# Optimization experiments

Hardware: AMD Instinct MI355X
Metric: run time of the kernel (lower is better)

Reference implementation:

```python
import jax, jax.numpy as jnp
import numpy as np

B, C, H, W = 4, 512, 64, 64
KEY_DIM, VALUE_DIM = 512, 512


def setup_inputs() -> dict:
    key = jax.random.key(0)
    k1, k2, k3, k4 = jax.random.split(key, 4)
    s = 1.0 / np.sqrt(C).astype(np.float32)
    x = jax.random.normal(k1, (B, C, H, W), jnp.float32)
    # torch nn.Linear weights have shape (out_features, in_features)
    Wk = jax.random.normal(k2, (KEY_DIM, C), jnp.float32) * s
    Wq = jax.random.normal(k3, (KEY_DIM, C), jnp.float32) * s
    Wv = jax.random.normal(k4, (VALUE_DIM, C), jnp.float32) * s
    return {"x": x, "Wk": Wk, "Wq": Wq, "Wv": Wv}


def reference(x, Wk, Wq, Wv):
    b, c, h, w = x.shape
    kd = Wk.shape[0]
    n = h * w
    # (b,c,h,w) -> (b, n, c) tokens, matching transpose+flatten in the original
    xt = x.transpose(0, 2, 3, 1).reshape(b, n, c)
    q = xt @ Wq.T  # (b, n, kd)
    k = xt @ Wk.T  # (b, n, kd)
    v = xt @ Wv.T  # (b, n, vd)
    scaling = np.sqrt(float(kd)).astype(np.float32)
    scores = jax.nn.softmax(jnp.einsum('bnd,bmd->bnm', q, k) / scaling, axis=-1)
    # original: output[j] = sum_i values[i] * scores[j, i]  ==  scores @ V
    out = jnp.einsum('bnm,bmv->bnv', scores, v)  # (b, n, vd)
    # original scores_out: sum over dim=0 (query index) of the (n, n) score matrix
    scores_out = scores.sum(axis=1).reshape(b, 1, h, w)
    out = out.reshape(b, h, w, -1).transpose(0, 3, 1, 2)  # (b, vd, h, w)
    return out, scores_out
```

## Files before the change

### kernel.cpp

```cpp
#include <hip/hip_runtime.h>


typedef short bf16x8 __attribute__((ext_vector_type(8)));
typedef float f32x4 __attribute__((ext_vector_type(4)));

#define NTOK 4096
#define DDIM 512
#define NB   4

__device__ __forceinline__ unsigned short f32_bf16(float f) {
  union { float f; unsigned u; } v; v.f = f;
  unsigned r = v.u + 0x7FFFu + ((v.u >> 16) & 1u);
  return (unsigned short)(r >> 16);
}

__device__ __forceinline__ float bf16_f32(short s) {
  union { unsigned u; float f; } v;
  v.u = ((unsigned)(unsigned short)s) << 16;
  return v.f;
}

__device__ __forceinline__ void gload_lds16(const unsigned short* g,
                                            unsigned short* l) {
  __builtin_amdgcn_global_load_lds(
      (__attribute__((address_space(1))) void*)(g),
      (__attribute__((address_space(3))) void*)(l), 16, 0, 0);
}

__global__ __launch_bounds__(256, 4) void qkv_proj(
    const float* __restrict__ x,
    const float* __restrict__ Wq,
    const float* __restrict__ Wk,
    const float* __restrict__ Wv,
    unsigned short* __restrict__ Qt,
    unsigned short* __restrict__ Kf,
    unsigned short* __restrict__ Vt)
{
  const int nt0 = blockIdx.x * 64;
  const int d0  = blockIdx.y * 64;
  const int b   = blockIdx.z;
  const int tid = threadIdx.x;
  const int wave = tid >> 6;
  const int lane = tid & 63;
  const int l15  = lane & 15;
  const int quad = lane >> 4;

  __shared__ __align__(16) unsigned short Xt[64 * 40];
  __shared__ __align__(16) unsigned short Wl[3][64 * 40];

  f32x4 aq[4], ak[4], av[4];
#pragma unroll
  for (int i = 0; i < 4; ++i) {
    aq[i] = (f32x4){0.f,0.f,0.f,0.f};
    ak[i] = (f32x4){0.f,0.f,0.f,0.f};
    av[i] = (f32x4){0.f,0.f,0.f,0.f};
  }

  const float* xb = x + (size_t)b * DDIM * NTOK + nt0;
  const int xn  = tid & 63;
  const int xc8 = tid >> 6;
  const int wc8 = tid & 3;
  const int wdd = tid >> 2;

  for (int cc = 0; cc < DDIM; cc += 32) {
    __syncthreads();
    {
      bf16x8 t;
#pragma unroll
      for (int j = 0; j < 8; ++j)
        t[j] = (short)f32_bf16(xb[(size_t)(cc + xc8 * 8 + j) * NTOK + xn]);
      *(bf16x8*)(&Xt[xn * 40 + xc8 * 8]) = t;
    }
    {
      const float* wsrc[3] = {Wq, Wk, Wv};
#pragma unroll
      for (int m = 0; m < 3; ++m) {
        const float* src = wsrc[m] + (size_t)(d0 + wdd) * DDIM + cc + wc8 * 8;
        bf16x8 t;
#pragma unroll
        for (int j = 0; j < 8; ++j) t[j] = (short)f32_bf16(src[j]);
        *(bf16x8*)(&Wl[m][wdd * 40 + wc8 * 8]) = t;
      }
    }
    __syncthreads();

    bf16x8 xa  = *(const bf16x8*)(&Xt[(wave * 16 + l15) * 40 + quad * 8]);
    bf16x8 wva = *(const bf16x8*)(&Wl[2][(wave * 16 + l15) * 40 + quad * 8]);
#pragma unroll
    for (int nt = 0; nt < 4; ++nt) {
      bf16x8 wqf = *(const bf16x8*)(&Wl[0][(nt * 16 + l15) * 40 + quad * 8]);
      bf16x8 wkf = *(const bf16x8*)(&Wl[1][(nt * 16 + l15) * 40 + quad * 8]);
      bf16x8 xbf = *(const bf16x8*)(&Xt[(nt * 16 + l15) * 40 + quad * 8]);
      aq[nt] = __builtin_amdgcn_mfma_f32_16x16x32_bf16(xa,  wqf, aq[nt], 0, 0, 0);
      ak[nt] = __builtin_amdgcn_mfma_f32_16x16x32_bf16(xa,  wkf, ak[nt], 0, 0, 0);
      av[nt] = __builtin_amdgcn_mfma_f32_16x16x32_bf16(wva, xbf, av[nt], 0, 0, 0);
    }
  }

#pragma unroll
  for (int nt = 0; nt < 4; ++nt) {
#pragma unroll
    for (int r = 0; r < 4; ++r) {
      const int tokq = nt0 + wave * 16 + quad * 4 + r;
      const int dq   = d0 + nt * 16 + l15;
      Qt[((size_t)b * NTOK + tokq) * DDIM + dq] = f32_bf16(aq[nt][r]);
      {
        const int kblk  = (nt0 >> 4) + wave;
        const int dc    = (d0 >> 5) + (nt >> 1);
        const int laneK = ((nt & 1) * 2 + (l15 >> 3)) * 16 + quad * 4 + r;
        Kf[((size_t)(b * 256 + kblk) * 16 + dc) * 512 + laneK * 8 + (l15 & 7)] =
            f32_bf16(ak[nt][r]);
      }
      const int dblk  = (d0 >> 4) + wave;
      const int ic    = (nt0 >> 5) + (nt >> 1);
      const int laneV = ((nt & 1) * 2 + (l15 >> 3)) * 16 + quad * 4 + r;
      Vt[(size_t)b * DDIM * NTOK +
         ((size_t)(dblk * 128 + ic) * 64 + laneV) * 8 + (l15 & 7)] =
          f32_bf16(av[nt][r]);
    }
  }
}

#define SCALE 0.044194173824159216f

__global__ __launch_bounds__(256, 2) void attn_lsum_p(
    const unsigned short* __restrict__ Qt,
    const unsigned short* __restrict__ Kf,
    unsigned short* __restrict__ Pt,
    float* __restrict__ lsum_g)
{
  const int qb = blockIdx.x;
  const int kp = blockIdx.y;
  const int b  = blockIdx.z;
  const int tid  = threadIdx.x;
  const int wave = tid >> 6;
  const int lane = tid & 63;
  const int l15  = lane & 15;
  const int quad = lane >> 4;
  const int q0   = qb * 128 + wave * 32;

  __shared__ __align__(16) unsigned short Klds[2][16384];

  bf16x8 qf[2][16];
#pragma unroll
  for (int qt = 0; qt < 2; ++qt) {
    const unsigned short* qp =
        Qt + ((size_t)b * NTOK + q0 + qt * 16 + l15) * DDIM + quad * 8;
#pragma unroll
    for (int dc = 0; dc < 16; ++dc) qf[qt][dc] = *(const bf16x8*)(qp + dc * 32);
  }

  unsigned short* Pq = Pt + (size_t)b * NTOK * NTOK +
                       (size_t)(qb * 2 + (wave >> 1)) * 262144;
  const int ntb = (wave & 1) * 2;

  float ls[2][4] = {{0.f,0.f,0.f,0.f},{0.f,0.f,0.f,0.f}};

  const unsigned short* Ksrc0 = Kf + ((size_t)(b * 256 + kp * 64) * 16) * 512;

#define KSTAGE(KC_, B_)                                                        \
  do {                                                                         \
    const unsigned short* ks_ = Ksrc0 + (size_t)(KC_)*16384;                   \
    _Pragma("unroll") for (int c_ = 0; c_ < 8; ++c_) {                         \
      const int ch_ = c_ * 4 + wave;                                           \
      gload_lds16(ks_ + ch_ * 512 + lane * 8, &Klds[B_][ch_ * 512]);           \
    }                                                                          \
  } while (0)

  KSTAGE(0, 0);
  __syncthreads();

  for (int kc2 = 0; kc2 < 32; ++kc2) {
    const int cb = kc2 & 1;
    if (kc2 < 31) KSTAGE(kc2 + 1, cb ^ 1);

#pragma unroll
    for (int kt = 0; kt < 2; ++kt) {
      const int kabs = kp * 64 + kc2 * 2 + kt;
      f32x4 s0 = (f32x4){0.f,0.f,0.f,0.f};
      f32x4 s1 = (f32x4){0.f,0.f,0.f,0.f};
#pragma unroll
      for (int dc = 0; dc < 16; ++dc) {
        const bf16x8 kbf =
            *(const bf16x8*)(&Klds[cb][(kt * 16 + dc) * 512 + lane * 8]);
        s0 = __builtin_amdgcn_mfma_f32_16x16x32_bf16(qf[0][dc], kbf, s0, 0, 0, 0);
        s1 = __builtin_amdgcn_mfma_f32_16x16x32_bf16(qf[1][dc], kbf, s1, 0, 0, 0);
      }
      const int ic    = kabs >> 1;
      const int lt_hi = ((kabs & 1) * 2 + (l15 >> 3)) * 16;
      const int jj    = l15 & 7;
#pragma unroll
      for (int r = 0; r < 4; ++r) {
        const float e0 = __expf(s0[r] * SCALE);
        const float e1 = __expf(s1[r] * SCALE);
        ls[0][r] += e0;
        ls[1][r] += e1;
        Pq[((size_t)(ic * 4 + ntb) * 64 + lt_hi + quad * 4 + r) * 8 + jj] =
            f32_bf16(e0);
        Pq[((size_t)(ic * 4 + ntb + 1) * 64 + lt_hi + quad * 4 + r) * 8 + jj] =
            f32_bf16(e1);
      }
    }
    __syncthreads();
  }
#undef KSTAGE

#pragma unroll
  for (int qt = 0; qt < 2; ++qt)
#pragma unroll
    for (int r = 0; r < 4; ++r) {
      float v = ls[qt][r];
      v += __shfl_xor(v, 1);
      v += __shfl_xor(v, 2);
      v += __shfl_xor(v, 4);
      v += __shfl_xor(v, 8);
      if (l15 == 0)
        unsafeAtomicAdd(&lsum_g[(size_t)b * NTOK + q0 + qt * 16 + quad * 4 + r], v);
    }
}

__global__ __launch_bounds__(256, 4) void attn_pv(
    const unsigned short* __restrict__ Pt,
    const unsigned short* __restrict__ Vt,
    const float* __restrict__ lsum_g,
    float* __restrict__ out,
    float* __restrict__ scpart)
{
  const int g     = blockIdx.x;
  const int xcd   = g & 7;
  const int slot  = g >> 3;
  const int combo = (xcd << 1) | (slot >> 6);
  const int q0b   = slot & 63;
  const int dpart = combo & 3;
  const int b     = combo >> 2;
  const int tid  = threadIdx.x;
  const int wave = tid >> 6;
  const int lane = tid & 63;
  const int l15  = lane & 15;
  const int quad = lane >> 4;

  const int dblk0 = dpart * 8 + wave * 2;
  const unsigned short* Pq =
      Pt + (size_t)b * NTOK * NTOK + (size_t)q0b * 262144;
  const unsigned short* Vb =
      Vt + (size_t)b * DDIM * NTOK + lane * 8;
  float* scp = scpart + ((size_t)(b * 64 + q0b)) * NTOK;

  __shared__ __align__(16) unsigned short Plds[2][8192];

  float rlv[4];
#pragma unroll
  for (int nt = 0; nt < 4; ++nt)
    rlv[nt] = 1.0f / lsum_g[(size_t)b * NTOK + q0b * 64 + nt * 16 + l15];

  f32x4 o[2][4];
#pragma unroll
  for (int i = 0; i < 2; ++i)
#pragma unroll
    for (int j = 0; j < 4; ++j) o[i][j] = (f32x4){0.f,0.f,0.f,0.f};

  bf16x8 vA[2], vB[2];

#define LOADVN(D_, IC_)                                                        \
  do {                                                                         \
    _Pragma("unroll") for (int mt = 0; mt < 2; ++mt)                           \
      D_[mt] = *(const bf16x8*)(Vb + (size_t)(dblk0 + mt) * 65536 +            \
                                (size_t)(IC_)*512);                            \
  } while (0)

#define PSTAGE(S_, B_)                                                         \
  do {                                                                         \
    const unsigned short* ps_ = Pq + (size_t)(S_)*8192;                        \
    _Pragma("unroll") for (int c_ = 0; c_ < 4; ++c_) {                         \
      const int ch_ = c_ * 4 + wave;                                           \
      gload_lds16(ps_ + ch_ * 512 + lane * 8, &Plds[B_][ch_ * 512]);           \
    }                                                                          \
  } while (0)

  LOADVN(vA, 0);
  LOADVN(vB, 1);
  PSTAGE(0, 0);
  __syncthreads();

  for (int s = 0; s < 32; ++s) {
    const int cb = s & 1;
    if (s < 31) PSTAGE(s + 1, cb ^ 1);
    const bool own = ((s >> 3) == dpart);
#pragma unroll
    for (int i = 0; i < 4; ++i) {
      const int ic = s * 4 + i;
      bf16x8 pb[4];
#pragma unroll
      for (int nt = 0; nt < 4; ++nt)
        pb[nt] = *(const bf16x8*)(&Plds[cb][i * 2048 + nt * 512 + lane * 8]);
      if ((i & 1) == 0) {
#pragma unroll
        for (int mt = 0; mt < 2; ++mt)
#pragma unroll
          for (int nt = 0; nt < 4; ++nt)
            o[mt][nt] = __builtin_amdgcn_mfma_f32_16x16x32_bf16(
                vA[mt], pb[nt], o[mt][nt], 0, 0, 0);
        if (ic + 2 < 128) LOADVN(vA, ic + 2);
      } else {
#pragma unroll
        for (int mt = 0; mt < 2; ++mt)
#pragma unroll
          for (int nt = 0; nt < 4; ++nt)
            o[mt][nt] = __builtin_amdgcn_mfma_f32_16x16x32_bf16(
                vB[mt], pb[nt], o[mt][nt], 0, 0, 0);
        if (ic + 2 < 128) LOADVN(vB, ic + 2);
      }
      if (own) {
#pragma unroll
        for (int jo = 0; jo < 2; ++jo) {
          const int j = wave * 2 + jo;
          float c = 0.f;
#pragma unroll
          for (int nt = 0; nt < 4; ++nt)
            c = fmaf(bf16_f32(pb[nt][j]), rlv[nt], c);
          c += __shfl_xor(c, 1);
          c += __shfl_xor(c, 2);
          c += __shfl_xor(c, 4);
          c += __shfl_xor(c, 8);
          if (l15 == 0) scp[ic * 32 + quad * 8 + j] = c;
        }
      }
    }
    __syncthreads();
  }
#undef LOADVN
#undef PSTAGE

  float* ob = out + ((size_t)b * DDIM + dpart * 128 + wave * 32) * NTOK + q0b * 64;
#pragma unroll
  for (int mt = 0; mt < 2; ++mt)
#pragma unroll
    for (int nt = 0; nt < 4; ++nt)
#pragma unroll
      for (int r = 0; r < 4; ++r)
        ob[(size_t)(mt * 16 + quad * 4 + r) * NTOK + nt * 16 + l15] =
            o[mt][nt][r] * rlv[nt];
}

__global__ __launch_bounds__(256, 8) void colsum_reduce(
    const float* __restrict__ scpart,
    float* __restrict__ scores_out)
{
  const int b = blockIdx.y;
  const int i = blockIdx.x * 256 + threadIdx.x;
  const float* src = scpart + (size_t)b * 64 * NTOK + i;
  float s = 0.f;
#pragma unroll
  for (int q = 0; q < 64; ++q) s += src[(size_t)q * NTOK];
  scores_out[(size_t)b * NTOK + i] = s;
}

extern "C" void kernel_launch(void* const* d_in, const int* in_sizes, int n_in,
                              void* d_out, int out_size, void* d_ws, size_t ws_size,
                              hipStream_t stream) {
  const float* x  = (const float*)d_in[0];
  const float* Wk = (const float*)d_in[1];
  const float* Wq = (const float*)d_in[2];
  const float* Wv = (const float*)d_in[3];

  float* out = (float*)d_out;
  float* scores_out = out + (size_t)NB * DDIM * NTOK;

  const size_t mat_elems = (size_t)NB * NTOK * DDIM;
  unsigned short* Qt = (unsigned short*)d_ws;
  unsigned short* Kf = Qt + mat_elems;
  unsigned short* Vt = Kf + mat_elems;
  float* lbuf = (float*)(Vt + mat_elems);
  unsigned short* Pt = (unsigned short*)(lbuf + (size_t)NB * NTOK);
  float* scpart = (float*)(Pt + (size_t)NB * NTOK * NTOK);

  hipMemsetAsync(lbuf, 0, (size_t)NB * NTOK * sizeof(float), stream);

  dim3 g1(NTOK / 64, DDIM / 64, NB);
  qkv_proj<<<g1, 256, 0, stream>>>(x, Wq, Wk, Wv, Qt, Kf, Vt);

  dim3 g2(NTOK / 128, 4, NB);
  attn_lsum_p<<<g2, 256, 0, stream>>>(Qt, Kf, Pt, lbuf);

  attn_pv<<<dim3(1024), 256, 0, stream>>>(Pt, Vt, lbuf, out, scpart);

  colsum_reduce<<<dim3(NTOK / 256, NB), 256, 0, stream>>>(scpart, scores_out);
}
```

Before: 355.2 us.

## Pre-convert inputs to bf16 token-major buffers and hoist column-sum out of PV loop

Adds a conversion kernel that transposes x to token-major bf16 and converts the weights to bf16 once, staging both in the P scratch buffer. The QKV projection then uses vectorized 16-byte loads instead of strided fp32 loads with per-element conversion, and no longer re-converts the weights in every block. In the PV kernel, the score column-sum is moved into a separate loop after the MFMA loop, which re-reads P from LDS, so the MFMA loop carries no conditional work. The cost is an extra launch and an extra pass over x through memory.

```diff
diff --git a/kernel.cpp b/kernel.cpp
--- a/kernel.cpp
+++ b/kernel.cpp
@@ -27,11 +27,62 @@
       (__attribute__((address_space(3))) void*)(l), 16, 0, 0);
 }
 
-__global__ __launch_bounds__(256, 4) void qkv_proj(
+__global__ __launch_bounds__(256, 4) void conv_bf16(
     const float* __restrict__ x,
     const float* __restrict__ Wq,
     const float* __restrict__ Wk,
     const float* __restrict__ Wv,
+    unsigned short* __restrict__ Xb,
+    unsigned short* __restrict__ Wb)
+{
+  const int bid = blockIdx.x;
+  const int tid = threadIdx.x;
+  if (bid < 2048) {
+    const int b  = bid >> 9;
+    const int t  = bid & 511;
+    const int c0 = (t >> 6) * 64;
+    const int n0 = (t & 63) * 64;
+    __shared__ __align__(16) unsigned short T[64][72];
+    const int cr = tid >> 2;
+    const int cg = tid & 3;
+    const float* src = x + ((size_t)b * DDIM + c0 + cr) * NTOK + n0 + cg * 16;
+    float v[16];
+#pragma unroll
+    for (int e4 = 0; e4 < 4; ++e4) {
+      const float4 a = *(const float4*)(src + e4 * 4);
+      v[e4 * 4 + 0] = a.x; v[e4 * 4 + 1] = a.y;
+      v[e4 * 4 + 2] = a.z; v[e4 * 4 + 3] = a.w;
+    }
+#pragma unroll
+    for (int e = 0; e < 16; ++e) T[cg * 16 + e][cr] = f32_bf16(v[e]);
+    __syncthreads();
+    const int nr  = tid >> 2;
+    const int cg2 = tid & 3;
+    unsigned short* dst =
+        Xb + ((size_t)b * NTOK + n0 + nr) * DDIM + c0 + cg2 * 16;
+    *(bf16x8*)(dst)     = *(const bf16x8*)(&T[nr][cg2 * 16]);
+    *(bf16x8*)(dst + 8) = *(const bf16x8*)(&T[nr][cg2 * 16 + 8]);
+  } else {
+    const int widx = bid - 2048;
+    const int m    = widx >> 7;
+    const float* wsrc[3] = {Wq, Wk, Wv};
+    const float* src = wsrc[m] + (size_t)(widx & 127) * 2048;
+    unsigned short* dst = Wb + (size_t)m * 262144 + (size_t)(widx & 127) * 2048;
+    const size_t i = (size_t)tid * 8;
+    const float4 a = *(const float4*)(src + i);
+    const float4 c = *(const float4*)(src + i + 4);
+    bf16x8 tv;
+    tv[0] = (short)f32_bf16(a.x); tv[1] = (short)f32_bf16(a.y);
+    tv[2] = (short)f32_bf16(a.z); tv[3] = (short)f32_bf16(a.w);
+    tv[4] = (short)f32_bf16(c.x); tv[5] = (short)f32_bf16(c.y);
+    tv[6] = (short)f32_bf16(c.z); tv[7] = (short)f32_bf16(c.w);
+    *(bf16x8*)(dst + i) = tv;
+  }
+}
+
+__global__ __launch_bounds__(256, 4) void qkv_proj(
+    const unsigned short* __restrict__ Xb,
+    const unsigned short* __restrict__ Wb,
     unsigned short* __restrict__ Qt,
     unsigned short* __restrict__ Kf,
     unsigned short* __restrict__ Vt)
@@ -56,31 +107,21 @@
     av[i] = (f32x4){0.f,0.f,0.f,0.f};
   }
 
-  const float* xb = x + (size_t)b * DDIM * NTOK + nt0;
-  const int xn  = tid & 63;
-  const int xc8 = tid >> 6;
+  const unsigned short* xb = Xb + ((size_t)b * NTOK + nt0) * DDIM;
+  const int tr  = tid >> 2;
+  const int cgx = tid & 3;
   const int wc8 = tid & 3;
   const int wdd = tid >> 2;
 
   for (int cc = 0; cc < DDIM; cc += 32) {
     __syncthreads();
-    {
-      bf16x8 t;
-#pragma unroll
-      for (int j = 0; j < 8; ++j)
-        t[j] = (short)f32_bf16(xb[(size_t)(cc + xc8 * 8 + j) * NTOK + xn]);
-      *(bf16x8*)(&Xt[xn * 40 + xc8 * 8]) = t;
-    }
-    {
-      const float* wsrc[3] = {Wq, Wk, Wv};
-#pragma unroll
-      for (int m = 0; m < 3; ++m) {
-        const float* src = wsrc[m] + (size_t)(d0 + wdd) * DDIM + cc + wc8 * 8;
-        bf16x8 t;
-#pragma unroll
-        for (int j = 0; j < 8; ++j) t[j] = (short)f32_bf16(src[j]);
-        *(bf16x8*)(&Wl[m][wdd * 40 + wc8 * 8]) = t;
-      }
+    *(bf16x8*)(&Xt[tr * 40 + cgx * 8]) =
+        *(const bf16x8*)(xb + (size_t)tr * DDIM + cc + cgx * 8);
+#pragma unroll
+    for (int m = 0; m < 3; ++m) {
+      const bf16x8 t = *(const bf16x8*)(
+          Wb + (size_t)m * 262144 + (size_t)(d0 + wdd) * 512 + cc + wc8 * 8);
+      *(bf16x8*)(&Wl[m][wdd * 40 + wc8 * 8]) = t;
     }
     __syncthreads();
 
@@ -285,7 +326,6 @@
   for (int s = 0; s < 32; ++s) {
     const int cb = s & 1;
     if (s < 31) PSTAGE(s + 1, cb ^ 1);
-    const bool own = ((s >> 3) == dpart);
 #pragma unroll
     for (int i = 0; i < 4; ++i) {
       const int ic = s * 4 + i;
@@ -310,14 +350,22 @@
                 vB[mt], pb[nt], o[mt][nt], 0, 0, 0);
         if (ic + 2 < 128) LOADVN(vB, ic + 2);
       }
-      if (own) {
+    }
+    if ((s >> 3) == dpart) {
+#pragma unroll
+      for (int i = 0; i < 4; ++i) {
+        const int ic = s * 4 + i;
+        bf16x8 pb2[4];
+#pragma unroll
+        for (int nt = 0; nt < 4; ++nt)
+          pb2[nt] = *(const bf16x8*)(&Plds[cb][i * 2048 + nt * 512 + lane * 8]);
 #pragma unroll
         for (int jo = 0; jo < 2; ++jo) {
           const int j = wave * 2 + jo;
           float c = 0.f;
 #pragma unroll
           for (int nt = 0; nt < 4; ++nt)
-            c = fmaf(bf16_f32(pb[nt][j]), rlv[nt], c);
+            c = fmaf(bf16_f32(pb2[nt][j]), rlv[nt], c);
           c += __shfl_xor(c, 1);
           c += __shfl_xor(c, 2);
           c += __shfl_xor(c, 4);
@@ -374,10 +422,15 @@
   unsigned short* Pt = (unsigned short*)(lbuf + (size_t)NB * NTOK);
   float* scpart = (float*)(Pt + (size_t)NB * NTOK * NTOK);
 
+  unsigned short* Xb = Pt;
+  unsigned short* Wb = Pt + mat_elems;
+
   hipMemsetAsync(lbuf, 0, (size_t)NB * NTOK * sizeof(float), stream);
 
+  conv_bf16<<<dim3(2432), 256, 0, stream>>>(x, Wq, Wk, Wv, Xb, Wb);
+
   dim3 g1(NTOK / 64, DDIM / 64, NB);
-  qkv_proj<<<g1, 256, 0, stream>>>(x, Wq, Wk, Wv, Qt, Kf, Vt);
+  qkv_proj<<<g1, 256, 0, stream>>>(Xb, Wb, Qt, Kf, Vt);
 
   dim3 g2(NTOK / 128, 4, NB);
   attn_lsum_p<<<g2, 256, 0, stream>>>(Qt, Kf, Pt, lbuf);
```

Measured after the change: 482.3 us. +35.8%, slower.
